# Optimization experiments

Hardware: AMD Instinct MI355X
Metric: run time of the kernel (lower is better)

Reference implementation:

```python
import jax, jax.numpy as jnp
import numpy as np

B, T, D, H = 8, 2048, 2048, 128  # batch, seq_len, d_model, head_size
NEG = -1e9


def setup_inputs() -> dict:
    key = jax.random.key(0)
    k0, k1, k2, k3 = jax.random.split(key, 4)
    x = jax.random.normal(k0, (B, T, D), dtype=jnp.float32)
    s = 1.0 / np.sqrt(D)
    Wq = jax.random.normal(k1, (D, H), dtype=jnp.float32) * s
    Wk = jax.random.normal(k2, (D, H), dtype=jnp.float32) * s
    Wv = jax.random.normal(k3, (D, H), dtype=jnp.float32) * s
    return {"x": x, "Wq": Wq, "Wk": Wk, "Wv": Wv}


def reference(x, Wq, Wk, Wv):
    # projections: [B,T,H]
    q = jnp.einsum('btd,dh->bth', x, Wq)
    k = jnp.einsum('btd,dh->bth', x, Wk)
    v = jnp.einsum('btd,dh->bth', x, Wv)
    # NOTE: module multiplies by sqrt(head_size) (faithful to source)
    wei = jnp.einsum('bqh,bkh->bqk', q, k) * jnp.sqrt(jnp.float32(H))
    causal = jnp.tril(jnp.ones((T, T), dtype=bool))
    wei = jnp.where(causal, wei, jnp.float32(NEG))
    wei = jax.nn.softmax(wei, axis=-1)
    # dropout is identity (deterministic=True / rate=0)
    out = jnp.einsum('bqk,bkh->bqh', wei, v)
    return out
```

## Files before the change

### kernel.cpp

```cpp
#include <hip/hip_runtime.h>
#include <math.h>

#define B_ 8
#define T_ 2048
#define D_ 2048
#define H_ 128
#define M_ (B_ * T_)

typedef __bf16 bf16x8 __attribute__((ext_vector_type(8)));
typedef __bf16 bf16x4 __attribute__((ext_vector_type(4)));
typedef float f32x4 __attribute__((ext_vector_type(4)));

#define MFMA(a, b, c) __builtin_amdgcn_mfma_f32_16x16x32_bf16(a, b, c, 0, 0, 0)

#define QH_OFF 0
#define QL_OFF (1 * 2097152)
#define KH_OFF (2 * 2097152)
#define KL_OFF (3 * 2097152)
#define VT_OFF (4 * 2097152)
#define WTH_OFF (5 * 2097152)
#define WTL_OFF (WTH_OFF + 786432)

__global__ __launch_bounds__(256) void prep_kernel(
    const float* __restrict__ Wq, const float* __restrict__ Wk,
    const float* __restrict__ Wv, __bf16* __restrict__ wt_hi,
    __bf16* __restrict__ wt_lo) {
  const int z = blockIdx.y;
  const int k0 = blockIdx.x * 64;
  const float* W = z == 0 ? Wq : z == 1 ? Wk : Wv;
  __shared__ float tile[64][132];
  const int t = threadIdx.x;
#pragma unroll
  for (int it = 0; it < 8; ++it) {
    int f4 = it * 256 + t;
    int row = f4 >> 5, c = (f4 & 31) << 2;
    *(float4*)&tile[row][c] = *(const float4*)&W[(size_t)(k0 + row) * H_ + c];
  }
  __syncthreads();
  int n = t >> 1, kh = (t & 1) << 5;
  __bf16 h[32], l[32];
#pragma unroll
  for (int kk = 0; kk < 32; ++kk) {
    float x = tile[kh + kk][n];
    __bf16 hi = (__bf16)x;
    h[kk] = hi;
    l[kk] = (__bf16)(x - (float)hi);
  }
  size_t base = (size_t)(z * H_ + n) * D_ + k0 + kh;
#pragma unroll
  for (int c = 0; c < 4; ++c) {
    *(bf16x8*)&wt_hi[base + c * 8] = *(bf16x8*)&h[c * 8];
    *(bf16x8*)&wt_lo[base + c * 8] = *(bf16x8*)&l[c * 8];
  }
}

#define WSTR 36
#define XSTR 72

__global__ __launch_bounds__(512, 2) void proj_kernel(
    const float* __restrict__ X, const __bf16* __restrict__ wt_hi,
    const __bf16* __restrict__ wt_lo, __bf16* __restrict__ qh,
    __bf16* __restrict__ ql, __bf16* __restrict__ kh,
    __bf16* __restrict__ kl, __bf16* __restrict__ vt) {
  __shared__ __align__(16) __bf16 Wh[384 * WSTR];
  __shared__ __align__(16) __bf16 Wl[384 * WSTR];
  __shared__ __align__(16) __bf16 Xs[64 * XSTR];
  const int t = threadIdx.x;
  const int wv = t >> 6, lane = t & 63;
  const int l15 = lane & 15, quad = lane >> 4, q8 = quad * 8;
  const int m0 = blockIdx.x * 64;
  const int nb = wv * 48;
  const int xm = t >> 3, xk = (t & 7) << 2;
  const float* xgp = X + (size_t)(m0 + xm) * D_ + xk;
  f32x4 acc[4][3] = {};
  float4 xr = *(const float4*)xgp;
  bf16x8 whr[3], wlr[3];
#pragma unroll
  for (int p = 0; p < 3; ++p) {
    int c = t + (p << 9);
    int n = c >> 2, o = (c & 3) << 3;
    whr[p] = *(const bf16x8*)(wt_hi + (size_t)n * D_ + o);
    wlr[p] = *(const bf16x8*)(wt_lo + (size_t)n * D_ + o);
  }
  for (int ks = 0; ks < 64; ++ks) {
    __syncthreads();
    {
      __bf16 h0 = (__bf16)xr.x, h1 = (__bf16)xr.y, h2 = (__bf16)xr.z,
             h3 = (__bf16)xr.w;
      bf16x4 hv = {h0, h1, h2, h3};
      bf16x4 lv = {(__bf16)(xr.x - (float)h0), (__bf16)(xr.y - (float)h1),
                   (__bf16)(xr.z - (float)h2), (__bf16)(xr.w - (float)h3)};
      *(bf16x4*)&Xs[xm * XSTR + xk] = hv;
      *(bf16x4*)&Xs[xm * XSTR + 32 + xk] = lv;
    }
#pragma unroll
    for (int p = 0; p < 3; ++p) {
      int c = t + (p << 9);
      int n = c >> 2, o = (c & 3) << 3;
      bf16x4 a, b, cc, d;
#pragma unroll
      for (int j = 0; j < 4; ++j) {
        a[j] = whr[p][j];
        b[j] = whr[p][j + 4];
        cc[j] = wlr[p][j];
        d[j] = wlr[p][j + 4];
      }
      *(bf16x4*)&Wh[n * WSTR + o] = a;
      *(bf16x4*)&Wh[n * WSTR + o + 4] = b;
      *(bf16x4*)&Wl[n * WSTR + o] = cc;
      *(bf16x4*)&Wl[n * WSTR + o + 4] = d;
    }
    if (ks < 63) {
      const int ko = (ks + 1) << 5;
      xr = *(const float4*)(xgp + ko);
#pragma unroll
      for (int p = 0; p < 3; ++p) {
        int c = t + (p << 9);
        int n = c >> 2, o = (c & 3) << 3;
        whr[p] = *(const bf16x8*)(wt_hi + (size_t)n * D_ + ko + o);
        wlr[p] = *(const bf16x8*)(wt_lo + (size_t)n * D_ + ko + o);
      }
    }
    __syncthreads();
    bf16x8 ah[4], al[4];
#pragma unroll
    for (int mg = 0; mg < 4; ++mg) {
      ah[mg] = *(bf16x8*)&Xs[(mg * 16 + l15) * XSTR + q8];
      al[mg] = *(bf16x8*)&Xs[(mg * 16 + l15) * XSTR + 32 + q8];
    }
#pragma unroll
    for (int nt = 0; nt < 3; ++nt) {
      const int n = nb + nt * 16 + l15;
      bf16x4 b0 = *(bf16x4*)&Wh[n * WSTR + q8];
      bf16x4 b1 = *(bf16x4*)&Wh[n * WSTR + q8 + 4];
      bf16x4 b2 = *(bf16x4*)&Wl[n * WSTR + q8];
      bf16x4 b3 = *(bf16x4*)&Wl[n * WSTR + q8 + 4];
      bf16x8 bh, bl;
#pragma unroll
      for (int j = 0; j < 4; ++j) {
        bh[j] = b0[j];
        bh[j + 4] = b1[j];
        bl[j] = b2[j];
        bl[j + 4] = b3[j];
      }
#pragma unroll
      for (int mg = 0; mg < 4; ++mg) {
        acc[mg][nt] = MFMA(ah[mg], bh, acc[mg][nt]);
        acc[mg][nt] = MFMA(al[mg], bh, acc[mg][nt]);
        acc[mg][nt] = MFMA(ah[mg], bl, acc[mg][nt]);
      }
    }
  }
#pragma unroll
  for (int nt = 0; nt < 3; ++nt) {
    int ncb = nb + nt * 16;
    int z = ncb >> 7;
    int h = (ncb & 127) + l15;
#pragma unroll
    for (int mg = 0; mg < 4; ++mg) {
      int r0 = m0 + mg * 16 + quad * 4;
      if (z == 2) {
        int b = m0 >> 11;
        int tt0 = (m0 & 2047) + mg * 16 + quad * 4;
        bf16x4 pv = {(__bf16)acc[mg][nt][0], (__bf16)acc[mg][nt][1],
                     (__bf16)acc[mg][nt][2], (__bf16)acc[mg][nt][3]};
        *(bf16x4*)&vt[(size_t)(b * H_ + h) * T_ + tt0] = pv;
      } else {
        __bf16* dh = z == 0 ? qh : kh;
        __bf16* dl = z == 0 ? ql : kl;
#pragma unroll
        for (int reg = 0; reg < 4; ++reg) {
          float v = acc[mg][nt][reg];
          __bf16 hi = (__bf16)v;
          dh[(size_t)(r0 + reg) * H_ + h] = hi;
          dl[(size_t)(r0 + reg) * H_ + h] = (__bf16)(v - (float)hi);
        }
      }
    }
  }
}

__global__ __launch_bounds__(512, 2) void attn_kernel(
    const __bf16* __restrict__ qh, const __bf16* __restrict__ qlo,
    const __bf16* __restrict__ kh, const __bf16* __restrict__ klo,
    const __bf16* __restrict__ vt, float* __restrict__ out) {
  const int t = threadIdx.x;
  const int wv = t >> 6, st = wv >> 2, cw = wv & 3;
  const int lane = t & 63, l15 = lane & 15, quad = lane >> 4;
  const int j = blockIdx.x, b = j & 7, pi = j >> 3;
  const int qlidx = (st == 0) ? pi : 63 - pi;
  const int t0 = qlidx * 32;
  const int nkt = (qlidx >> 1) + 1;
  __shared__ __align__(16) __bf16 Pbuf[8][32 * 72];
  __shared__ __align__(16) float Obuf[2][32 * 132];
  __shared__ float mlb[2][4][32], llb[2][4][32];
  const size_t qrow0 = (size_t)b * T_ + t0;
  bf16x8 qfh[2][4], qfl[2][4];
#pragma unroll
  for (int mg = 0; mg < 2; ++mg)
#pragma unroll
    for (int ds = 0; ds < 4; ++ds) {
      size_t off = (qrow0 + mg * 16 + l15) * H_ + ds * 32 + quad * 8;
      qfh[mg][ds] = *(const bf16x8*)(qh + off);
      qfl[mg][ds] = *(const bf16x8*)(qlo + off);
    }
  f32x4 O[2][8] = {};
  float ms[2][4], ls[2][4];
#pragma unroll
  for (int mg = 0; mg < 2; ++mg)
#pragma unroll
    for (int reg = 0; reg < 4; ++reg) {
      ms[mg][reg] = -INFINITY;
      ls[mg][reg] = 0.f;
    }
  const __bf16* vtb = vt + (size_t)b * H_ * T_;
  const float scale = 11.313708498984761f;
  for (int kt_i = cw; kt_i < nkt; kt_i += 4) {
    const int kt = kt_i * 64;
    f32x4 S[2][4] = {};
#pragma unroll
    for (int ds = 0; ds < 4; ++ds)
#pragma unroll
      for (int ct = 0; ct < 4; ++ct) {
        size_t koff =
            ((size_t)b * T_ + kt + ct * 16 + l15) * H_ + ds * 32 + quad * 8;
        bf16x8 bh = *(const bf16x8*)(kh + koff);
        bf16x8 bl = *(const bf16x8*)(klo + koff);
#pragma unroll
        for (int mg = 0; mg < 2; ++mg) {
          S[mg][ct] = MFMA(qfh[mg][ds], bh, S[mg][ct]);
          S[mg][ct] = MFMA(qfl[mg][ds], bh, S[mg][ct]);
          S[mg][ct] = MFMA(qfh[mg][ds], bl, S[mg][ct]);
        }
      }
    const bool diag = (kt_i == nkt - 1);
#pragma unroll
    for (int mg = 0; mg < 2; ++mg)
#pragma unroll
      for (int ct = 0; ct < 4; ++ct)
#pragma unroll
        for (int reg = 0; reg < 4; ++reg) {
          float s = S[mg][ct][reg] * scale;
          if (diag && (kt + ct * 16 + l15 > t0 + mg * 16 + quad * 4 + reg))
            s = -1e30f;
          S[mg][ct][reg] = s;
        }
    float al_[2][4];
#pragma unroll
    for (int mg = 0; mg < 2; ++mg)
#pragma unroll
      for (int reg = 0; reg < 4; ++reg) {
        float r = fmaxf(fmaxf(S[mg][0][reg], S[mg][1][reg]),
                        fmaxf(S[mg][2][reg], S[mg][3][reg]));
        r = fmaxf(r, __shfl_xor(r, 1));
        r = fmaxf(r, __shfl_xor(r, 2));
        r = fmaxf(r, __shfl_xor(r, 4));
        r = fmaxf(r, __shfl_xor(r, 8));
        float mn = fmaxf(ms[mg][reg], r);
        float a = __expf(ms[mg][reg] - mn);
        ms[mg][reg] = mn;
        float ps = 0.f;
#pragma unroll
        for (int ct = 0; ct < 4; ++ct) {
          float p = __expf(S[mg][ct][reg] - mn);
          S[mg][ct][reg] = p;
          ps += p;
        }
        ps += __shfl_xor(ps, 1);
        ps += __shfl_xor(ps, 2);
        ps += __shfl_xor(ps, 4);
        ps += __shfl_xor(ps, 8);
        ls[mg][reg] = ls[mg][reg] * a + ps;
        al_[mg][reg] = a;
      }
#pragma unroll
    for (int mg = 0; mg < 2; ++mg)
#pragma unroll
      for (int ht = 0; ht < 8; ++ht)
#pragma unroll
        for (int reg = 0; reg < 4; ++reg) O[mg][ht][reg] *= al_[mg][reg];
#pragma unroll
    for (int mg = 0; mg < 2; ++mg)
#pragma unroll
      for (int ct = 0; ct < 4; ++ct)
#pragma unroll
        for (int reg = 0; reg < 4; ++reg)
          Pbuf[wv][(mg * 16 + quad * 4 + reg) * 72 + ct * 16 + l15] =
              (__bf16)S[mg][ct][reg];
#pragma unroll
    for (int ks = 0; ks < 2; ++ks) {
      bf16x8 pf0 = *(bf16x8*)&Pbuf[wv][(l15)*72 + ks * 32 + quad * 8];
      bf16x8 pf1 = *(bf16x8*)&Pbuf[wv][(16 + l15) * 72 + ks * 32 + quad * 8];
#pragma unroll
      for (int ht = 0; ht < 8; ++ht) {
        bf16x8 vf = *(const bf16x8*)&vtb[(size_t)(ht * 16 + l15) * T_ + kt +
                                         ks * 32 + quad * 8];
        O[0][ht] = MFMA(pf0, vf, O[0][ht]);
        O[1][ht] = MFMA(pf1, vf, O[1][ht]);
      }
    }
  }
  if (l15 == 0) {
#pragma unroll
    for (int mg = 0; mg < 2; ++mg)
#pragma unroll
      for (int reg = 0; reg < 4; ++reg) {
        mlb[st][cw][mg * 16 + quad * 4 + reg] = ms[mg][reg];
        llb[st][cw][mg * 16 + quad * 4 + reg] = ls[mg][reg];
      }
  }
  for (int i = t; i < 2 * 32 * 132; i += 512) ((float*)Obuf)[i] = 0.f;
  __syncthreads();
  float aw[2][4];
#pragma unroll
  for (int mg = 0; mg < 2; ++mg)
#pragma unroll
    for (int reg = 0; reg < 4; ++reg) {
      int row = mg * 16 + quad * 4 + reg;
      float M = fmaxf(fmaxf(mlb[st][0][row], mlb[st][1][row]),
                      fmaxf(mlb[st][2][row], mlb[st][3][row]));
      float L = 0.f;
#pragma unroll
      for (int w = 0; w < 4; ++w)
        L += llb[st][w][row] * __expf(mlb[st][w][row] - M);
      aw[mg][reg] = __expf(ms[mg][reg] - M) / L;
    }
#pragma unroll
  for (int mg = 0; mg < 2; ++mg)
#pragma unroll
    for (int ht = 0; ht < 8; ++ht)
#pragma unroll
      for (int reg = 0; reg < 4; ++reg)
        atomicAdd(&Obuf[st][(mg * 16 + quad * 4 + reg) * 132 + ht * 16 + l15],
                  O[mg][ht][reg] * aw[mg][reg]);
  __syncthreads();
  {
    const int stw = t >> 8, tt = t & 255;
    const int qlw = (stw == 0) ? pi : 63 - pi;
    const size_t obase = ((size_t)b * T_ + qlw * 32) * H_;
#pragma unroll
    for (int i = 0; i < 4; ++i) {
      int f4 = i * 256 + tt;
      int row = f4 >> 5, c = (f4 & 31) << 2;
      *(float4*)&out[obase + (size_t)row * H_ + c] =
          *(float4*)&Obuf[stw][row * 132 + c];
    }
  }
}

extern "C" void kernel_launch(void* const* d_in, const int* in_sizes, int n_in,
                              void* d_out, int out_size, void* d_ws, size_t ws_size,
                              hipStream_t stream) {
  const float* x = (const float*)d_in[0];
  const float* Wq = (const float*)d_in[1];
  const float* Wk = (const float*)d_in[2];
  const float* Wv = (const float*)d_in[3];
  __bf16* ws = (__bf16*)d_ws;
  float* out = (float*)d_out;
  prep_kernel<<<dim3(32, 3), 256, 0, stream>>>(Wq, Wk, Wv, ws + WTH_OFF,
                                               ws + WTL_OFF);
  proj_kernel<<<256, 512, 0, stream>>>(x, ws + WTH_OFF, ws + WTL_OFF,
                                       ws + QH_OFF, ws + QL_OFF, ws + KH_OFF,
                                       ws + KL_OFF, ws + VT_OFF);
  attn_kernel<<<256, 512, 0, stream>>>(ws + QH_OFF, ws + QL_OFF, ws + KH_OFF,
                                       ws + KL_OFF, ws + VT_OFF, out);
}
```

Before: 382.8 us.

## Split projection GEMM across two column halves to double block count

The projection kernel now launches 512 blocks, each computing 64 rows by 192 of the 384 fused Q/K/V output columns, with warps arranged as a 2x4 grid instead of 8 column strips. This halves the shared-memory weight tile and per-thread accumulators, so occupancy can rise (launch bounds now 4 blocks/CU) and the 256 CUs all get work. The cost is that each X tile is loaded and split into hi/lo twice, once per column half, which adds global traffic and conversion work.

```diff
diff --git a/kernel.cpp b/kernel.cpp
--- a/kernel.cpp
+++ b/kernel.cpp
@@ -57,31 +57,39 @@
 #define WSTR 36
 #define XSTR 72
 
-__global__ __launch_bounds__(512, 2) void proj_kernel(
+__global__ __launch_bounds__(512, 4) void proj_kernel(
     const float* __restrict__ X, const __bf16* __restrict__ wt_hi,
     const __bf16* __restrict__ wt_lo, __bf16* __restrict__ qh,
     __bf16* __restrict__ ql, __bf16* __restrict__ kh,
     __bf16* __restrict__ kl, __bf16* __restrict__ vt) {
-  __shared__ __align__(16) __bf16 Wh[384 * WSTR];
-  __shared__ __align__(16) __bf16 Wl[384 * WSTR];
+  __shared__ __align__(16) __bf16 Wh[192 * WSTR];
+  __shared__ __align__(16) __bf16 Wl[192 * WSTR];
   __shared__ __align__(16) __bf16 Xs[64 * XSTR];
   const int t = threadIdx.x;
   const int wv = t >> 6, lane = t & 63;
   const int l15 = lane & 15, quad = lane >> 4, q8 = quad * 8;
-  const int m0 = blockIdx.x * 64;
-  const int nb = wv * 48;
+  const int bi = blockIdx.x;
+  const int m0 = (bi >> 1) * 64;
+  const int nbase = (bi & 1) * 192;
+  const int wr = wv >> 2, wc = wv & 3;
   const int xm = t >> 3, xk = (t & 7) << 2;
   const float* xgp = X + (size_t)(m0 + xm) * D_ + xk;
-  f32x4 acc[4][3] = {};
-  float4 xr = *(const float4*)xgp;
-  bf16x8 whr[3], wlr[3];
+  const __bf16* wsrc[3];
+  __bf16* wdst[3];
 #pragma unroll
   for (int p = 0; p < 3; ++p) {
     int c = t + (p << 9);
-    int n = c >> 2, o = (c & 3) << 3;
-    whr[p] = *(const bf16x8*)(wt_hi + (size_t)n * D_ + o);
-    wlr[p] = *(const bf16x8*)(wt_lo + (size_t)n * D_ + o);
-  }
+    int sel = c >= 768;
+    int cr = sel ? c - 768 : c;
+    int r = cr >> 2, o = (c & 3) << 3;
+    wsrc[p] = (sel ? wt_lo : wt_hi) + (size_t)(nbase + r) * D_ + o;
+    wdst[p] = (sel ? Wl : Wh) + r * WSTR + o;
+  }
+  f32x4 acc[2][3] = {};
+  float4 xr = *(const float4*)xgp;
+  bf16x8 wreg[3];
+#pragma unroll
+  for (int p = 0; p < 3; ++p) wreg[p] = *(const bf16x8*)wsrc[p];
   for (int ks = 0; ks < 64; ++ks) {
     __syncthreads();
     {
@@ -95,42 +103,32 @@
     }
 #pragma unroll
     for (int p = 0; p < 3; ++p) {
-      int c = t + (p << 9);
-      int n = c >> 2, o = (c & 3) << 3;
-      bf16x4 a, b, cc, d;
+      bf16x4 a, b;
 #pragma unroll
       for (int j = 0; j < 4; ++j) {
-        a[j] = whr[p][j];
-        b[j] = whr[p][j + 4];
-        cc[j] = wlr[p][j];
-        d[j] = wlr[p][j + 4];
-      }
-      *(bf16x4*)&Wh[n * WSTR + o] = a;
-      *(bf16x4*)&Wh[n * WSTR + o + 4] = b;
-      *(bf16x4*)&Wl[n * WSTR + o] = cc;
-      *(bf16x4*)&Wl[n * WSTR + o + 4] = d;
+        a[j] = wreg[p][j];
+        b[j] = wreg[p][j + 4];
+      }
+      *(bf16x4*)(wdst[p]) = a;
+      *(bf16x4*)(wdst[p] + 4) = b;
     }
     if (ks < 63) {
       const int ko = (ks + 1) << 5;
       xr = *(const float4*)(xgp + ko);
 #pragma unroll
-      for (int p = 0; p < 3; ++p) {
-        int c = t + (p << 9);
-        int n = c >> 2, o = (c & 3) << 3;
-        whr[p] = *(const bf16x8*)(wt_hi + (size_t)n * D_ + ko + o);
-        wlr[p] = *(const bf16x8*)(wt_lo + (size_t)n * D_ + ko + o);
-      }
+      for (int p = 0; p < 3; ++p)
+        wreg[p] = *(const bf16x8*)(wsrc[p] + ko);
     }
     __syncthreads();
-    bf16x8 ah[4], al[4];
-#pragma unroll
-    for (int mg = 0; mg < 4; ++mg) {
-      ah[mg] = *(bf16x8*)&Xs[(mg * 16 + l15) * XSTR + q8];
-      al[mg] = *(bf16x8*)&Xs[(mg * 16 + l15) * XSTR + 32 + q8];
+    bf16x8 ah[2], al[2];
+#pragma unroll
+    for (int mg = 0; mg < 2; ++mg) {
+      ah[mg] = *(bf16x8*)&Xs[(wr * 32 + mg * 16 + l15) * XSTR + q8];
+      al[mg] = *(bf16x8*)&Xs[(wr * 32 + mg * 16 + l15) * XSTR + 32 + q8];
     }
 #pragma unroll
     for (int nt = 0; nt < 3; ++nt) {
-      const int n = nb + nt * 16 + l15;
+      const int n = wc * 48 + nt * 16 + l15;
       bf16x4 b0 = *(bf16x4*)&Wh[n * WSTR + q8];
       bf16x4 b1 = *(bf16x4*)&Wh[n * WSTR + q8 + 4];
       bf16x4 b2 = *(bf16x4*)&Wl[n * WSTR + q8];
@@ -144,7 +142,7 @@
         bl[j + 4] = b3[j];
       }
 #pragma unroll
-      for (int mg = 0; mg < 4; ++mg) {
+      for (int mg = 0; mg < 2; ++mg) {
         acc[mg][nt] = MFMA(ah[mg], bh, acc[mg][nt]);
         acc[mg][nt] = MFMA(al[mg], bh, acc[mg][nt]);
         acc[mg][nt] = MFMA(ah[mg], bl, acc[mg][nt]);
@@ -153,15 +151,15 @@
   }
 #pragma unroll
   for (int nt = 0; nt < 3; ++nt) {
-    int ncb = nb + nt * 16;
+    int ncb = nbase + wc * 48 + nt * 16;
     int z = ncb >> 7;
     int h = (ncb & 127) + l15;
 #pragma unroll
-    for (int mg = 0; mg < 4; ++mg) {
-      int r0 = m0 + mg * 16 + quad * 4;
+    for (int mg = 0; mg < 2; ++mg) {
+      int r0 = m0 + wr * 32 + mg * 16 + quad * 4;
       if (z == 2) {
         int b = m0 >> 11;
-        int tt0 = (m0 & 2047) + mg * 16 + quad * 4;
+        int tt0 = (m0 & 2047) + wr * 32 + mg * 16 + quad * 4;
         bf16x4 pv = {(__bf16)acc[mg][nt][0], (__bf16)acc[mg][nt][1],
                      (__bf16)acc[mg][nt][2], (__bf16)acc[mg][nt][3]};
         *(bf16x4*)&vt[(size_t)(b * H_ + h) * T_ + tt0] = pv;
@@ -359,7 +357,7 @@
   float* out = (float*)d_out;
   prep_kernel<<<dim3(32, 3), 256, 0, stream>>>(Wq, Wk, Wv, ws + WTH_OFF,
                                                ws + WTL_OFF);
-  proj_kernel<<<256, 512, 0, stream>>>(x, ws + WTH_OFF, ws + WTL_OFF,
+  proj_kernel<<<512, 512, 0, stream>>>(x, ws + WTH_OFF, ws + WTL_OFF,
                                        ws + QH_OFF, ws + QL_OFF, ws + KH_OFF,
                                        ws + KL_OFF, ws + VT_OFF);
   attn_kernel<<<256, 512, 0, stream>>>(ws + QH_OFF, ws + QL_OFF, ws + KH_OFF,
```

Result: no change. 377.4 us (-1.4%).
